# Performance work log

Hardware: AMD Instinct MI355X
Metric: run time of the kernel (lower is better)

Reference implementation:

```python
import jax, jax.numpy as jnp
import numpy as np

D_MODEL = 1024
D_FF = 4096
N_EXPERTS = 8
TOP_K = 2
B, T = 4, 2048


def setup_inputs() -> dict:
    key = jax.random.key(0)
    ks = jax.random.split(key, 5)
    x = jax.random.normal(ks[0], (B, T, D_MODEL), dtype=jnp.float32)
    def lin(k, shape, fan_in):
        return jax.random.normal(k, shape, dtype=jnp.float32) / np.float32(np.sqrt(fan_in))
    return {
        "x": x,
        "router_w": lin(ks[1], (N_EXPERTS, D_MODEL), D_MODEL),          # router: Linear(D,E), no bias
        "w_gate": lin(ks[2], (N_EXPERTS, D_MODEL, D_FF), D_MODEL),      # per-expert gate proj
        "w_up": lin(ks[3], (N_EXPERTS, D_MODEL, D_FF), D_MODEL),        # per-expert up proj
        "w_down": lin(ks[4], (N_EXPERTS, D_FF, D_MODEL), D_FF),         # per-expert down proj
    }


def reference(x, router_w, w_gate, w_up, w_down):
    Bx, Tx, D = x.shape
    xf = x.reshape(-1, D)                              # [N, D]
    logits = xf @ router_w.T                           # [N, E]
    scores = jax.nn.softmax(logits, axis=-1)
    topk_scores, topk_ids = jax.lax.top_k(scores, TOP_K)          # [N, K]
    topk_scores = topk_scores / topk_scores.sum(-1, keepdims=True)
    # combine weight per (token, expert): sum over k of normalized score where routed
    cw = (jax.nn.one_hot(topk_ids, N_EXPERTS, dtype=xf.dtype) * topk_scores[..., None]).sum(1)  # [N, E]

    # scan over experts: dense SwiGLU on all tokens, weighted combine.
    # Mathematically identical to the masked gather/scatter loop (zero-weight tokens
    # contribute zero); keeps shapes static and memory bounded per expert.
    def body(acc, inputs):
        wg, wu, wd, w = inputs                         # wg/wu:[D,F], wd:[F,D], w:[N]
        h = jax.nn.silu(xf @ wg) * (xf @ wu)           # [N, F]
        acc = acc + w[:, None] * (h @ wd)              # [N, D]
        return acc, None

    out, _ = jax.lax.scan(body, jnp.zeros_like(xf), (w_gate, w_up, w_down, cw.T))
    return out.reshape(Bx, Tx, D)
```

## Files before the change

### kernel.cpp

```cpp
#include <hip/hip_runtime.h>
#include <hip/hip_bf16.h>
#include <stdint.h>

#define D_MODEL 1024
#define D_FF    4096
#define NEXP    8
#define NTOK    8192
#define NSLOT   16384

typedef __bf16 bf16x8 __attribute__((ext_vector_type(8)));
typedef float  f32x4  __attribute__((ext_vector_type(4)));
typedef unsigned short us8 __attribute__((ext_vector_type(8)));
typedef unsigned short us4 __attribute__((ext_vector_type(4)));

#define OFF_XB   0ull
#define OFF_WGT  16777216ull
#define OFF_WUT  83886080ull
#define OFF_WDT  150994944ull
#define OFF_H    218103808ull
#define OFF_TOKE 352321536ull
#define OFF_TOKW 352387072ull
#define OFF_ROWT 352452608ull
#define OFF_WGTL 352518144ull
#define OFF_CNT  352583680ull
#define OFF_OFFS 352583744ull
#define OFF_FILL 352583808ull

__device__ __forceinline__ unsigned short f2b(float f) {
  union { float f; unsigned int u; } v; v.f = f;
  unsigned int r = (v.u + 0x7FFFu + ((v.u >> 16) & 1u)) >> 16;
  return (unsigned short)r;
}

__device__ __forceinline__ f32x4 MFMA(bf16x8 a, bf16x8 b, f32x4 c) {
  return __builtin_amdgcn_mfma_f32_16x16x32_bf16(a, b, c, 0, 0, 0);
}

__device__ __forceinline__ void GLL16(const void* g, void* l) {
  __builtin_amdgcn_global_load_lds(
      (__attribute__((address_space(1))) void*)g,
      (__attribute__((address_space(3))) void*)l, 16, 0, 0);
}

__global__ __launch_bounds__(256) void k_cvt_x(const float* __restrict__ x,
                                               unsigned short* __restrict__ xb) {
  size_t i = ((size_t)blockIdx.x * 256 + threadIdx.x) * 8;
  float4 a = *(const float4*)(x + i);
  float4 b = *(const float4*)(x + i + 4);
  us8 o;
  o[0]=f2b(a.x); o[1]=f2b(a.y); o[2]=f2b(a.z); o[3]=f2b(a.w);
  o[4]=f2b(b.x); o[5]=f2b(b.y); o[6]=f2b(b.z); o[7]=f2b(b.w);
  *(us8*)(xb + i) = o;
}

__global__ __launch_bounds__(256) void k_tc(const float* __restrict__ in,
                                            unsigned short* __restrict__ out,
                                            int R, int C) {
  __shared__ float t[64][65];
  int e = blockIdx.z;
  int r0 = blockIdx.y * 64, c0 = blockIdx.x * 64;
  const float* src = in + (size_t)e * R * C;
  unsigned short* dst = out + (size_t)e * R * C;
  int tid = threadIdx.x;
  int lr = tid >> 4;
  int lc = (tid & 15) * 4;
#pragma unroll
  for (int i = 0; i < 4; ++i) {
    float4 v = *(const float4*)(src + (size_t)(r0 + lr + 16 * i) * C + c0 + lc);
    t[lr + 16 * i][lc + 0] = v.x;
    t[lr + 16 * i][lc + 1] = v.y;
    t[lr + 16 * i][lc + 2] = v.z;
    t[lr + 16 * i][lc + 3] = v.w;
  }
  __syncthreads();
#pragma unroll
  for (int i = 0; i < 4; ++i) {
    int c = lr + 16 * i;
    us4 o;
    o[0] = f2b(t[lc + 0][c]);
    o[1] = f2b(t[lc + 1][c]);
    o[2] = f2b(t[lc + 2][c]);
    o[3] = f2b(t[lc + 3][c]);
    *(us4*)(dst + (size_t)(c0 + c) * R + r0 + lc) = o;
  }
}

__global__ __launch_bounds__(256) void k_router(const float* __restrict__ x,
                                                const float* __restrict__ rw,
                                                int* __restrict__ tok_e,
                                                float* __restrict__ tok_w,
                                                int* __restrict__ counts) {
  int w = threadIdx.x >> 6, l = threadIdx.x & 63;
  int t = blockIdx.x * 4 + w;
  const float* xr = x + (size_t)t * D_MODEL + l * 16;
  float4 xa = *(const float4*)(xr);
  float4 xb4 = *(const float4*)(xr + 4);
  float4 xc = *(const float4*)(xr + 8);
  float4 xd = *(const float4*)(xr + 12);
  float lg[NEXP];
#pragma unroll
  for (int e = 0; e < NEXP; ++e) {
    const float* wr = rw + e * D_MODEL + l * 16;
    float4 wa = *(const float4*)(wr);
    float4 wb = *(const float4*)(wr + 4);
    float4 wc = *(const float4*)(wr + 8);
    float4 wd4 = *(const float4*)(wr + 12);
    float s = xa.x*wa.x + xa.y*wa.y + xa.z*wa.z + xa.w*wa.w
            + xb4.x*wb.x + xb4.y*wb.y + xb4.z*wb.z + xb4.w*wb.w
            + xc.x*wc.x + xc.y*wc.y + xc.z*wc.z + xc.w*wc.w
            + xd.x*wd4.x + xd.y*wd4.y + xd.z*wd4.z + xd.w*wd4.w;
#pragma unroll
    for (int o = 32; o; o >>= 1) s += __shfl_xor(s, o, 64);
    lg[e] = s;
  }
  if (l == 0) {
    int e1 = 0; float l1 = lg[0];
#pragma unroll
    for (int e = 1; e < NEXP; ++e) if (lg[e] > l1) { l1 = lg[e]; e1 = e; }
    int e2 = -1; float l2 = -3.4e38f;
#pragma unroll
    for (int e = 0; e < NEXP; ++e) if (e != e1 && lg[e] > l2) { l2 = lg[e]; e2 = e; }
    float w1 = 1.f / (1.f + expf(l2 - l1));
    tok_e[2 * t] = e1; tok_e[2 * t + 1] = e2;
    tok_w[2 * t] = w1; tok_w[2 * t + 1] = 1.f - w1;
    atomicAdd(&counts[e1], 1);
    atomicAdd(&counts[e2], 1);
  }
}

__global__ void k_scan(const int* __restrict__ counts, int* __restrict__ offs) {
  if (threadIdx.x == 0) {
    int s = 0;
#pragma unroll
    for (int e = 0; e < NEXP; ++e) { offs[e] = s; s += counts[e]; }
    offs[NEXP] = s;
  }
}

__global__ __launch_bounds__(256) void k_scatter(const int* __restrict__ tok_e,
                                                 const float* __restrict__ tok_w,
                                                 const int* __restrict__ offs,
                                                 int* __restrict__ fill,
                                                 int* __restrict__ rowtok,
                                                 float* __restrict__ wgtl) {
  int t = blockIdx.x * 256 + threadIdx.x;
#pragma unroll
  for (int k = 0; k < 2; ++k) {
    int e = tok_e[2 * t + k];
    int p = atomicAdd(&fill[e], 1);
    int s = offs[e] + p;
    rowtok[s] = t;
    wgtl[s] = tok_w[2 * t + k];
  }
}

__global__ __launch_bounds__(256, 2) void k_gateup(
    const unsigned short* __restrict__ xb,
    const unsigned short* __restrict__ wgT,
    const unsigned short* __restrict__ wuT,
    const int* __restrict__ rowtok,
    const int* __restrict__ offs,
    unsigned short* __restrict__ h) {
  int e = blockIdx.z;
  int eoff = offs[e];
  int cnt = offs[e + 1] - eoff;
  int m0 = blockIdx.y * 128;
  if (m0 >= cnt) return;
  int f0 = blockIdx.x * 128;

  __shared__ __align__(16) unsigned short lA[8192];
  __shared__ __align__(16) unsigned short lG[8192];
  __shared__ __align__(16) unsigned short lU[8192];

  int tid = threadIdx.x;
  int l = tid & 63, w = tid >> 6;
  int wm = w >> 1, wn = w & 1;
  int lrow = l & 15, lk = (l >> 4) * 8;
  int scol = (tid & 7) * 8;

  const unsigned short* wgp = wgT + (size_t)e * D_FF * D_MODEL;
  const unsigned short* wup = wuT + (size_t)e * D_FF * D_MODEL;

  const unsigned short* aptr[4];
  const unsigned short* gptr[4];
  const unsigned short* uptr[4];
#pragma unroll
  for (int r = 0; r < 4; ++r) {
    int mrow = m0 + (tid >> 3) + 32 * r;
    int srow = rowtok[eoff + (mrow < cnt ? mrow : cnt - 1)];
    aptr[r] = xb + (size_t)srow * D_MODEL + scol;
    int frow = f0 + (tid >> 3) + 32 * r;
    gptr[r] = wgp + (size_t)frow * D_MODEL + scol;
    uptr[r] = wup + (size_t)frow * D_MODEL + scol;
  }

  f32x4 zero = {0.f, 0.f, 0.f, 0.f};
  f32x4 ag[4][4], au[4][4];
#pragma unroll
  for (int i = 0; i < 4; ++i)
#pragma unroll
    for (int j = 0; j < 4; ++j) { ag[i][j] = zero; au[i][j] = zero; }

  unsigned short* lAw = lA + w * 512;
  unsigned short* lGw = lG + w * 512;
  unsigned short* lUw = lU + w * 512;

  for (int ks = 0; ks < 16; ++ks) {
    int k0 = ks * 64;
    __syncthreads();
#pragma unroll
    for (int r = 0; r < 4; ++r) {
      GLL16(aptr[r] + k0, lAw + r * 2048);
      GLL16(gptr[r] + k0, lGw + r * 2048);
      GLL16(uptr[r] + k0, lUw + r * 2048);
    }
    __syncthreads();
#pragma unroll
    for (int kk = 0; kk < 2; ++kk) {
      bf16x8 av[4], gv[4], uv[4];
#pragma unroll
      for (int i = 0; i < 4; ++i) {
        av[i] = *(const bf16x8*)&lA[(wm * 64 + i * 16 + lrow) * 64 + kk * 32 + lk];
        gv[i] = *(const bf16x8*)&lG[(wn * 64 + i * 16 + lrow) * 64 + kk * 32 + lk];
        uv[i] = *(const bf16x8*)&lU[(wn * 64 + i * 16 + lrow) * 64 + kk * 32 + lk];
      }
#pragma unroll
      for (int mi = 0; mi < 4; ++mi)
#pragma unroll
        for (int ni = 0; ni < 4; ++ni) {
          ag[mi][ni] = MFMA(av[mi], gv[ni], ag[mi][ni]);
          au[mi][ni] = MFMA(av[mi], uv[ni], au[mi][ni]);
        }
    }
  }

#pragma unroll
  for (int mi = 0; mi < 4; ++mi) {
#pragma unroll
    for (int j = 0; j < 4; ++j) {
      int row = wm * 64 + mi * 16 + (l >> 4) * 4 + j;
      if (m0 + row < cnt) {
        size_t hb = (size_t)(eoff + m0 + row) * D_FF + f0;
#pragma unroll
        for (int ni = 0; ni < 4; ++ni) {
          int col = wn * 64 + ni * 16 + (l & 15);
          float g = ag[mi][ni][j];
          float u = au[mi][ni][j];
          float s = g / (1.f + __expf(-g)) * u;
          h[hb + col] = f2b(s);
        }
      }
    }
  }
}

__global__ __launch_bounds__(256, 2) void k_down(
    const unsigned short* __restrict__ h,
    const unsigned short* __restrict__ wdT,
    const int* __restrict__ rowtok,
    const float* __restrict__ wgtl,
    const int* __restrict__ offs,
    float* __restrict__ out) {
  int e = blockIdx.z;
  int eoff = offs[e];
  int cnt = offs[e + 1] - eoff;
  int m0 = blockIdx.y * 128;
  if (m0 >= cnt) return;
  int d0 = blockIdx.x * 128;

  __shared__ __align__(16) unsigned short lA[8192];
  __shared__ __align__(16) unsigned short lB[8192];

  int tid = threadIdx.x;
  int l = tid & 63, w = tid >> 6;
  int wm = w >> 1, wn = w & 1;
  int lrow = l & 15, lk = (l >> 4) * 8;
  int scol = (tid & 7) * 8;

  const unsigned short* wdp = wdT + (size_t)e * D_MODEL * D_FF;
  const unsigned short* aptr[4];
  const unsigned short* bptr[4];
#pragma unroll
  for (int r = 0; r < 4; ++r) {
    int mrow = m0 + (tid >> 3) + 32 * r;
    aptr[r] = h + (size_t)(eoff + (mrow < cnt ? mrow : cnt - 1)) * D_FF + scol;
    bptr[r] = wdp + (size_t)(d0 + (tid >> 3) + 32 * r) * D_FF + scol;
  }

  f32x4 zero = {0.f, 0.f, 0.f, 0.f};
  f32x4 ac[4][4];
#pragma unroll
  for (int i = 0; i < 4; ++i)
#pragma unroll
    for (int j = 0; j < 4; ++j) ac[i][j] = zero;

  unsigned short* lAw = lA + w * 512;
  unsigned short* lBw = lB + w * 512;

  for (int ks = 0; ks < 64; ++ks) {
    int k0 = ks * 64;
    __syncthreads();
#pragma unroll
    for (int r = 0; r < 4; ++r) {
      GLL16(aptr[r] + k0, lAw + r * 2048);
      GLL16(bptr[r] + k0, lBw + r * 2048);
    }
    __syncthreads();
#pragma unroll
    for (int kk = 0; kk < 2; ++kk) {
      bf16x8 av[4], bv[4];
#pragma unroll
      for (int i = 0; i < 4; ++i) {
        av[i] = *(const bf16x8*)&lA[(wm * 64 + i * 16 + lrow) * 64 + kk * 32 + lk];
        bv[i] = *(const bf16x8*)&lB[(wn * 64 + i * 16 + lrow) * 64 + kk * 32 + lk];
      }
#pragma unroll
      for (int mi = 0; mi < 4; ++mi)
#pragma unroll
        for (int ni = 0; ni < 4; ++ni)
          ac[mi][ni] = MFMA(av[mi], bv[ni], ac[mi][ni]);
    }
  }

#pragma unroll
  for (int mi = 0; mi < 4; ++mi) {
#pragma unroll
    for (int j = 0; j < 4; ++j) {
      int row = wm * 64 + mi * 16 + (l >> 4) * 4 + j;
      int grow = m0 + row;
      if (grow < cnt) {
        float wv = wgtl[eoff + grow];
        int tok = rowtok[eoff + grow];
        float* ob = out + (size_t)tok * D_MODEL + d0;
#pragma unroll
        for (int ni = 0; ni < 4; ++ni) {
          int col = wn * 64 + ni * 16 + (l & 15);
          atomicAdd(ob + col, ac[mi][ni][j] * wv);
        }
      }
    }
  }
}

extern "C" void kernel_launch(void* const* d_in, const int* in_sizes, int n_in,
                              void* d_out, int out_size, void* d_ws, size_t ws_size,
                              hipStream_t stream) {
  const float* x  = (const float*)d_in[0];
  const float* rw = (const float*)d_in[1];
  const float* wg = (const float*)d_in[2];
  const float* wu = (const float*)d_in[3];
  const float* wd = (const float*)d_in[4];
  float* out = (float*)d_out;
  char* ws = (char*)d_ws;

  unsigned short* xb  = (unsigned short*)(ws + OFF_XB);
  unsigned short* wgT = (unsigned short*)(ws + OFF_WGT);
  unsigned short* wuT = (unsigned short*)(ws + OFF_WUT);
  unsigned short* wdT = (unsigned short*)(ws + OFF_WDT);
  unsigned short* hb  = (unsigned short*)(ws + OFF_H);
  int*   tok_e  = (int*)(ws + OFF_TOKE);
  float* tok_w  = (float*)(ws + OFF_TOKW);
  int*   rowtok = (int*)(ws + OFF_ROWT);
  float* wgtl   = (float*)(ws + OFF_WGTL);
  int*   counts = (int*)(ws + OFF_CNT);
  int*   offs   = (int*)(ws + OFF_OFFS);
  int*   fill   = (int*)(ws + OFF_FILL);

  hipMemsetAsync(out, 0, (size_t)NTOK * D_MODEL * 4, stream);
  hipMemsetAsync(ws + OFF_CNT, 0, 192, stream);

  k_cvt_x<<<4096, 256, 0, stream>>>(x, xb);
  k_tc<<<dim3(64, 16, 8), 256, 0, stream>>>(wg, wgT, D_MODEL, D_FF);
  k_tc<<<dim3(64, 16, 8), 256, 0, stream>>>(wu, wuT, D_MODEL, D_FF);
  k_tc<<<dim3(16, 64, 8), 256, 0, stream>>>(wd, wdT, D_FF, D_MODEL);

  k_router<<<NTOK / 4, 256, 0, stream>>>(x, rw, tok_e, tok_w, counts);
  k_scan<<<1, 64, 0, stream>>>(counts, offs);
  k_scatter<<<NTOK / 256, 256, 0, stream>>>(tok_e, tok_w, offs, fill, rowtok, wgtl);

  k_gateup<<<dim3(32, 64, 8), 256, 0, stream>>>(xb, wgT, wuT, rowtok, offs, hb);
  k_down<<<dim3(8, 64, 8), 256, 0, stream>>>(hb, wdT, rowtok, wgtl, offs, out);
}
```

Baseline: 1.321 ms.

## Replace expert GEMMs with double-buffered 256x256 swizzled-LDS pipelined kernel

Introduces a templated 512-thread GEMM with 256x256 tiles, XOR-swizzled LDS layout and two-stage double buffering that prefetches the next K tiles while issuing MFMAs with raised wave priority. Gate and up projections become separate launches: the first stores the gate result to the h buffer, and the second reads it back to apply SwiGLU. The aim is to hide global load latency and cut LDS bank conflicts and barrier stalls. The cost is an extra read and write of the intermediate buffer, extra bf16 rounding of the gate, and large LDS use that limits occupancy.

```diff
diff --git a/kernel.cpp b/kernel.cpp
--- a/kernel.cpp
+++ b/kernel.cpp
@@ -31,6 +31,10 @@
   unsigned int r = (v.u + 0x7FFFu + ((v.u >> 16) & 1u)) >> 16;
   return (unsigned short)r;
 }
+__device__ __forceinline__ float b2f(unsigned short b) {
+  union { unsigned int u; float f; } v; v.u = ((unsigned int)b) << 16;
+  return v.f;
+}
 
 __device__ __forceinline__ f32x4 MFMA(bf16x8 a, bf16x8 b, f32x4 c) {
   return __builtin_amdgcn_mfma_f32_16x16x32_bf16(a, b, c, 0, 0, 0);
@@ -41,6 +45,10 @@
       (__attribute__((address_space(1))) void*)g,
       (__attribute__((address_space(3))) void*)l, 16, 0, 0);
 }
+
+#define BAR()  asm volatile("s_barrier" ::: "memory")
+#define VM8()  asm volatile("s_waitcnt vmcnt(8)" ::: "memory")
+#define VM0()  asm volatile("s_waitcnt vmcnt(0)" ::: "memory")
 
 __global__ __launch_bounds__(256) void k_cvt_x(const float* __restrict__ x,
                                                unsigned short* __restrict__ xb) {
@@ -154,192 +162,192 @@
   }
 }
 
-__global__ __launch_bounds__(256, 2) void k_gateup(
-    const unsigned short* __restrict__ xb,
-    const unsigned short* __restrict__ wgT,
-    const unsigned short* __restrict__ wuT,
+template<int MODE, int KDIM, int NB>
+__global__ __launch_bounds__(512, 2) void gemm8(
+    const unsigned short* __restrict__ Ag,
+    const unsigned short* __restrict__ Bg,
     const int* __restrict__ rowtok,
+    const float* __restrict__ wgtl,
     const int* __restrict__ offs,
-    unsigned short* __restrict__ h) {
+    unsigned short* __restrict__ hbuf,
+    float* __restrict__ out) {
+  constexpr int NKT = KDIM / 64;
   int e = blockIdx.z;
   int eoff = offs[e];
   int cnt = offs[e + 1] - eoff;
-  int m0 = blockIdx.y * 128;
+  int m0 = blockIdx.y * 256;
   if (m0 >= cnt) return;
-  int f0 = blockIdx.x * 128;
-
-  __shared__ __align__(16) unsigned short lA[8192];
-  __shared__ __align__(16) unsigned short lG[8192];
-  __shared__ __align__(16) unsigned short lU[8192];
+  int n0 = blockIdx.x * 256;
+
+  __shared__ __align__(16) unsigned short lds[65536];
+  char* ldsb = (char*)lds;
 
   int tid = threadIdx.x;
   int l = tid & 63, w = tid >> 6;
-  int wm = w >> 1, wn = w & 1;
-  int lrow = l & 15, lk = (l >> 4) * 8;
-  int scol = (tid & 7) * 8;
-
-  const unsigned short* wgp = wgT + (size_t)e * D_FF * D_MODEL;
-  const unsigned short* wup = wuT + (size_t)e * D_FF * D_MODEL;
-
-  const unsigned short* aptr[4];
-  const unsigned short* gptr[4];
-  const unsigned short* uptr[4];
-#pragma unroll
-  for (int r = 0; r < 4; ++r) {
-    int mrow = m0 + (tid >> 3) + 32 * r;
-    int srow = rowtok[eoff + (mrow < cnt ? mrow : cnt - 1)];
-    aptr[r] = xb + (size_t)srow * D_MODEL + scol;
-    int frow = f0 + (tid >> 3) + 32 * r;
-    gptr[r] = wgp + (size_t)frow * D_MODEL + scol;
-    uptr[r] = wup + (size_t)frow * D_MODEL + scol;
-  }
-
-  f32x4 zero = {0.f, 0.f, 0.f, 0.f};
-  f32x4 ag[4][4], au[4][4];
-#pragma unroll
-  for (int i = 0; i < 4; ++i)
-#pragma unroll
-    for (int j = 0; j < 4; ++j) { ag[i][j] = zero; au[i][j] = zero; }
-
-  unsigned short* lAw = lA + w * 512;
-  unsigned short* lGw = lG + w * 512;
-  unsigned short* lUw = lU + w * 512;
-
-  for (int ks = 0; ks < 16; ++ks) {
-    int k0 = ks * 64;
-    __syncthreads();
-#pragma unroll
-    for (int r = 0; r < 4; ++r) {
-      GLL16(aptr[r] + k0, lAw + r * 2048);
-      GLL16(gptr[r] + k0, lGw + r * 2048);
-      GLL16(uptr[r] + k0, lUw + r * 2048);
+  int wm = w >> 2, wn = w & 3;
+
+  int srow = tid >> 3;
+  int sslot = (tid & 7) ^ (srow & 7);
+  const unsigned short* aB[4];
+  const unsigned short* bB[4];
+  const unsigned short* Bexp = Bg + (size_t)e * (size_t)NB * KDIM;
+#pragma unroll
+  for (int h = 0; h < 2; ++h)
+#pragma unroll
+    for (int j = 0; j < 2; ++j) {
+      int r = m0 + h * 128 + j * 64 + srow;
+      int rc = r < cnt ? r : cnt - 1;
+      if (MODE < 2)
+        aB[h * 2 + j] = Ag + (size_t)rowtok[eoff + rc] * D_MODEL + sslot * 8;
+      else
+        aB[h * 2 + j] = Ag + (size_t)(eoff + rc) * D_FF + sslot * 8;
+      bB[h * 2 + j] = Bexp + (size_t)(n0 + h * 128 + j * 64 + srow) * KDIM + sslot * 8;
     }
-    __syncthreads();
-#pragma unroll
-    for (int kk = 0; kk < 2; ++kk) {
-      bf16x8 av[4], gv[4], uv[4];
-#pragma unroll
-      for (int i = 0; i < 4; ++i) {
-        av[i] = *(const bf16x8*)&lA[(wm * 64 + i * 16 + lrow) * 64 + kk * 32 + lk];
-        gv[i] = *(const bf16x8*)&lG[(wn * 64 + i * 16 + lrow) * 64 + kk * 32 + lk];
-        uv[i] = *(const bf16x8*)&lU[(wn * 64 + i * 16 + lrow) * 64 + kk * 32 + lk];
-      }
-#pragma unroll
-      for (int mi = 0; mi < 4; ++mi)
-#pragma unroll
-        for (int ni = 0; ni < 4; ++ni) {
-          ag[mi][ni] = MFMA(av[mi], gv[ni], ag[mi][ni]);
-          au[mi][ni] = MFMA(av[mi], uv[ni], au[mi][ni]);
-        }
-    }
-  }
-
-#pragma unroll
-  for (int mi = 0; mi < 4; ++mi) {
+
+#define STAGE_A(t, buf) {                                                  \
+    int k0 = (t) * 64;                                                     \
+    GLL16(aB[0] + k0, ldsb + (buf) * 65536 + 0 * 8192 + tid * 16);         \
+    GLL16(aB[1] + k0, ldsb + (buf) * 65536 + 1 * 8192 + tid * 16);         \
+    GLL16(aB[2] + k0, ldsb + (buf) * 65536 + 2 * 8192 + tid * 16);         \
+    GLL16(aB[3] + k0, ldsb + (buf) * 65536 + 3 * 8192 + tid * 16); }
+#define STAGE_B(t, buf) {                                                  \
+    int k0 = (t) * 64;                                                     \
+    GLL16(bB[0] + k0, ldsb + (buf) * 65536 + 32768 + 0 * 8192 + tid * 16); \
+    GLL16(bB[1] + k0, ldsb + (buf) * 65536 + 32768 + 1 * 8192 + tid * 16); \
+    GLL16(bB[2] + k0, ldsb + (buf) * 65536 + 32768 + 2 * 8192 + tid * 16); \
+    GLL16(bB[3] + k0, ldsb + (buf) * 65536 + 32768 + 3 * 8192 + tid * 16); }
+
+#define RDA(L, mi, kk) (*(const bf16x8*)((L) +                             \
+    (wm * 128 + (mi) * 16 + (l & 15)) * 128 +                              \
+    ((((l >> 4) + 4 * (kk)) ^ (l & 7)) * 16)))
+#define RDB(L, ni, kk) (*(const bf16x8*)((L) + 32768 +                     \
+    (wn * 64 + (ni) * 16 + (l & 15)) * 128 +                               \
+    ((((l >> 4) + 4 * (kk)) ^ (l & 7)) * 16)))
+
+  f32x4 acc[8][4];
+#pragma unroll
+  for (int i = 0; i < 8; ++i)
+#pragma unroll
+    for (int j = 0; j < 4; ++j) acc[i][j] = (f32x4){0.f, 0.f, 0.f, 0.f};
+
+  STAGE_A(0, 0); STAGE_B(0, 0);
+  STAGE_A(1, 1); STAGE_B(1, 1);
+  VM8();
+  BAR();
+
+  for (int t = 0; t < NKT; ++t) {
+    int cur = t & 1;
+    char* L = ldsb + cur * 65536;
+    bf16x8 aF[4][2], aF2[4][2], bF[2][2], bF2[2][2];
+
+#pragma unroll
+    for (int mi = 0; mi < 4; ++mi)
+#pragma unroll
+      for (int kk = 0; kk < 2; ++kk) aF[mi][kk] = RDA(L, mi, kk);
+#pragma unroll
+    for (int ni = 0; ni < 2; ++ni)
+#pragma unroll
+      for (int kk = 0; kk < 2; ++kk) bF[ni][kk] = RDB(L, ni, kk);
+    BAR();
+    __builtin_amdgcn_s_setprio(1);
+#pragma unroll
+    for (int mi = 0; mi < 4; ++mi)
+#pragma unroll
+      for (int ni = 0; ni < 2; ++ni)
+#pragma unroll
+        for (int kk = 0; kk < 2; ++kk)
+          acc[mi][ni] = MFMA(aF[mi][kk], bF[ni][kk], acc[mi][ni]);
+    __builtin_amdgcn_s_setprio(0);
+    BAR();
+
+#pragma unroll
+    for (int ni = 0; ni < 2; ++ni)
+#pragma unroll
+      for (int kk = 0; kk < 2; ++kk) bF2[ni][kk] = RDB(L, ni + 2, kk);
+    BAR();
+    __builtin_amdgcn_s_setprio(1);
+#pragma unroll
+    for (int mi = 0; mi < 4; ++mi)
+#pragma unroll
+      for (int ni = 0; ni < 2; ++ni)
+#pragma unroll
+        for (int kk = 0; kk < 2; ++kk)
+          acc[mi][ni + 2] = MFMA(aF[mi][kk], bF2[ni][kk], acc[mi][ni + 2]);
+    __builtin_amdgcn_s_setprio(0);
+    BAR();
+
+#pragma unroll
+    for (int mi = 0; mi < 4; ++mi)
+#pragma unroll
+      for (int kk = 0; kk < 2; ++kk) aF2[mi][kk] = RDA(L, mi + 4, kk);
+    if (t + 2 < NKT) STAGE_B(t + 2, cur);
+    BAR();
+    __builtin_amdgcn_s_setprio(1);
+#pragma unroll
+    for (int mi = 0; mi < 4; ++mi)
+#pragma unroll
+      for (int ni = 0; ni < 2; ++ni)
+#pragma unroll
+        for (int kk = 0; kk < 2; ++kk)
+          acc[mi + 4][ni] = MFMA(aF2[mi][kk], bF[ni][kk], acc[mi + 4][ni]);
+    __builtin_amdgcn_s_setprio(0);
+    BAR();
+
+    if (t + 2 < NKT) STAGE_A(t + 2, cur);
+    BAR();
+    __builtin_amdgcn_s_setprio(1);
+#pragma unroll
+    for (int mi = 0; mi < 4; ++mi)
+#pragma unroll
+      for (int ni = 0; ni < 2; ++ni)
+#pragma unroll
+        for (int kk = 0; kk < 2; ++kk)
+          acc[mi + 4][ni + 2] = MFMA(aF2[mi][kk], bF2[ni][kk], acc[mi + 4][ni + 2]);
+    __builtin_amdgcn_s_setprio(0);
+    if (t + 2 < NKT) { VM8(); } else { VM0(); }
+    BAR();
+  }
+
+#pragma unroll
+  for (int mi = 0; mi < 8; ++mi) {
 #pragma unroll
     for (int j = 0; j < 4; ++j) {
-      int row = wm * 64 + mi * 16 + (l >> 4) * 4 + j;
+      int row = wm * 128 + mi * 16 + (l >> 4) * 4 + j;
       if (m0 + row < cnt) {
-        size_t hb = (size_t)(eoff + m0 + row) * D_FF + f0;
-#pragma unroll
-        for (int ni = 0; ni < 4; ++ni) {
-          int col = wn * 64 + ni * 16 + (l & 15);
-          float g = ag[mi][ni][j];
-          float u = au[mi][ni][j];
-          float s = g / (1.f + __expf(-g)) * u;
-          h[hb + col] = f2b(s);
+        int grow = eoff + m0 + row;
+        if (MODE == 0) {
+          size_t base = (size_t)grow * D_FF + n0;
+#pragma unroll
+          for (int ni = 0; ni < 4; ++ni) {
+            int col = wn * 64 + ni * 16 + (l & 15);
+            hbuf[base + col] = f2b(acc[mi][ni][j]);
+          }
+        } else if (MODE == 1) {
+          size_t base = (size_t)grow * D_FF + n0;
+#pragma unroll
+          for (int ni = 0; ni < 4; ++ni) {
+            int col = wn * 64 + ni * 16 + (l & 15);
+            float g = b2f(hbuf[base + col]);
+            float s = g / (1.f + __expf(-g)) * acc[mi][ni][j];
+            hbuf[base + col] = f2b(s);
+          }
+        } else {
+          float wv = wgtl[grow];
+          int tok = rowtok[grow];
+          float* ob = out + (size_t)tok * D_MODEL + n0;
+#pragma unroll
+          for (int ni = 0; ni < 4; ++ni) {
+            int col = wn * 64 + ni * 16 + (l & 15);
+            atomicAdd(ob + col, acc[mi][ni][j] * wv);
+          }
         }
       }
     }
   }
-}
-
-__global__ __launch_bounds__(256, 2) void k_down(
-    const unsigned short* __restrict__ h,
-    const unsigned short* __restrict__ wdT,
-    const int* __restrict__ rowtok,
-    const float* __restrict__ wgtl,
-    const int* __restrict__ offs,
-    float* __restrict__ out) {
-  int e = blockIdx.z;
-  int eoff = offs[e];
-  int cnt = offs[e + 1] - eoff;
-  int m0 = blockIdx.y * 128;
-  if (m0 >= cnt) return;
-  int d0 = blockIdx.x * 128;
-
-  __shared__ __align__(16) unsigned short lA[8192];
-  __shared__ __align__(16) unsigned short lB[8192];
-
-  int tid = threadIdx.x;
-  int l = tid & 63, w = tid >> 6;
-  int wm = w >> 1, wn = w & 1;
-  int lrow = l & 15, lk = (l >> 4) * 8;
-  int scol = (tid & 7) * 8;
-
-  const unsigned short* wdp = wdT + (size_t)e * D_MODEL * D_FF;
-  const unsigned short* aptr[4];
-  const unsigned short* bptr[4];
-#pragma unroll
-  for (int r = 0; r < 4; ++r) {
-    int mrow = m0 + (tid >> 3) + 32 * r;
-    aptr[r] = h + (size_t)(eoff + (mrow < cnt ? mrow : cnt - 1)) * D_FF + scol;
-    bptr[r] = wdp + (size_t)(d0 + (tid >> 3) + 32 * r) * D_FF + scol;
-  }
-
-  f32x4 zero = {0.f, 0.f, 0.f, 0.f};
-  f32x4 ac[4][4];
-#pragma unroll
-  for (int i = 0; i < 4; ++i)
-#pragma unroll
-    for (int j = 0; j < 4; ++j) ac[i][j] = zero;
-
-  unsigned short* lAw = lA + w * 512;
-  unsigned short* lBw = lB + w * 512;
-
-  for (int ks = 0; ks < 64; ++ks) {
-    int k0 = ks * 64;
-    __syncthreads();
-#pragma unroll
-    for (int r = 0; r < 4; ++r) {
-      GLL16(aptr[r] + k0, lAw + r * 2048);
-      GLL16(bptr[r] + k0, lBw + r * 2048);
-    }
-    __syncthreads();
-#pragma unroll
-    for (int kk = 0; kk < 2; ++kk) {
-      bf16x8 av[4], bv[4];
-#pragma unroll
-      for (int i = 0; i < 4; ++i) {
-        av[i] = *(const bf16x8*)&lA[(wm * 64 + i * 16 + lrow) * 64 + kk * 32 + lk];
-        bv[i] = *(const bf16x8*)&lB[(wn * 64 + i * 16 + lrow) * 64 + kk * 32 + lk];
-      }
-#pragma unroll
-      for (int mi = 0; mi < 4; ++mi)
-#pragma unroll
-        for (int ni = 0; ni < 4; ++ni)
-          ac[mi][ni] = MFMA(av[mi], bv[ni], ac[mi][ni]);
-    }
-  }
-
-#pragma unroll
-  for (int mi = 0; mi < 4; ++mi) {
-#pragma unroll
-    for (int j = 0; j < 4; ++j) {
-      int row = wm * 64 + mi * 16 + (l >> 4) * 4 + j;
-      int grow = m0 + row;
-      if (grow < cnt) {
-        float wv = wgtl[eoff + grow];
-        int tok = rowtok[eoff + grow];
-        float* ob = out + (size_t)tok * D_MODEL + d0;
-#pragma unroll
-        for (int ni = 0; ni < 4; ++ni) {
-          int col = wn * 64 + ni * 16 + (l & 15);
-          atomicAdd(ob + col, ac[mi][ni][j] * wv);
-        }
-      }
-    }
-  }
+#undef STAGE_A
+#undef STAGE_B
+#undef RDA
+#undef RDB
 }
 
 extern "C" void kernel_launch(void* const* d_in, const int* in_sizes, int n_in,
@@ -378,6 +386,7 @@
   k_scan<<<1, 64, 0, stream>>>(counts, offs);
   k_scatter<<<NTOK / 256, 256, 0, stream>>>(tok_e, tok_w, offs, fill, rowtok, wgtl);
 
-  k_gateup<<<dim3(32, 64, 8), 256, 0, stream>>>(xb, wgT, wuT, rowtok, offs, hb);
-  k_down<<<dim3(8, 64, 8), 256, 0, stream>>>(hb, wdT, rowtok, wgtl, offs, out);
-}
+  gemm8<0, D_MODEL, D_FF><<<dim3(16, 32, 8), 512, 0, stream>>>(xb, wgT, rowtok, wgtl, offs, hb, out);
+  gemm8<1, D_MODEL, D_FF><<<dim3(16, 32, 8), 512, 0, stream>>>(xb, wuT, rowtok, wgtl, offs, hb, out);
+  gemm8<2, D_FF, D_MODEL><<<dim3(4, 32, 8), 512, 0, stream>>>(hb, wdT, rowtok, wgtl, offs, hb, out);
+}
```

After: 1.332 ms. About the same (+0.9%).
